# Kernel optimization log

Hardware: AMD Instinct MI355X
Metric: run time of the kernel (lower is better)

Reference implementation:

```python
import jax, jax.numpy as jnp
import numpy as np
import math

T = 4194304          # sequence length (e.g. minute bars)
MAX_KERNEL = 700     # number of EMA taps (from init_alpha=0.01)
INIT_ALPHA = 0.01


def setup_inputs() -> dict:
    key = jax.random.key(0)
    x = jax.random.normal(key, (T,), dtype=jnp.float32)
    # learnable logit-space alpha parameter: sigmoid(w_alpha) = init_alpha
    w_alpha = jnp.float32(math.log(INIT_ALPHA / (1.0 - INIT_ALPHA)))
    return {"x": x, "w_alpha": w_alpha}


def reference(x, w_alpha):
    K = MAX_KERNEL
    alpha = jax.nn.sigmoid(w_alpha)
    # exponential-decay kernel w_k = alpha * (1-alpha)^k, reconstructed each forward
    k = jnp.arange(K, dtype=x.dtype)
    kernel = alpha * jnp.power(1.0 - alpha, k)          # [K]
    w = kernel[::-1].reshape(1, 1, K)                   # flipped, [O=1, I=1, K]
    # causal left-pad with the first sample replicated (as in the torch module)
    left_pad = jnp.full((K - 1,), x[0], dtype=x.dtype)
    x_padded = jnp.concatenate([left_pad, x])[None, None, :]  # [1,1,T+K-1]
    # torch F.conv1d is cross-correlation; lax conv is too -> same math
    out = jax.lax.conv_general_dilated(
        x_padded, w,
        window_strides=(1,), padding="VALID",
        dimension_numbers=("NCH", "OIH", "NCH"),
    )
    return out[0, 0]  # [T]
```

## Files before the change

### kernel.cpp

```cpp
#include <hip/hip_runtime.h>
#include <math.h>


#define K_TAPS 700
#define NB     4096
#define EXT    2560
#define TOTAL  (NB + EXT)
#define BLOCK  256
#define LSEG   (TOTAL / BLOCK)

__global__ __launch_bounds__(BLOCK)
void diffema_kernel(const float* __restrict__ x,
                    const float* __restrict__ w_alpha,
                    float* __restrict__ out,
                    int T) {
    __shared__ float xs[TOTAL];
    __shared__ float ys[TOTAL];
    __shared__ float wP[BLOCK / 64];
    __shared__ float wV[BLOCK / 64];

    const int tid = threadIdx.x;
    const int bid = blockIdx.x;
    const int t0  = bid * NB;
    const int base = t0 - EXT;

    const float w     = w_alpha[0];
    const float alpha = 1.0f / (1.0f + expf(-w));
    const float c     = 1.0f - alpha;
    const float cK    = powf(c, (float)K_TAPS);
    const float cL    = powf(c, (float)LSEG);

    for (int j = tid; j < TOTAL; j += BLOCK) {
        int p = base + j;
        if (p < 0) p = 0;
        xs[j] = x[p];
    }
    __syncthreads();

    const int s0 = tid * LSEG;
    float v = 0.0f;
#pragma unroll
    for (int j = 0; j < LSEG; ++j) {
        v = c * v + alpha * xs[s0 + j];
    }

    float P = cL, V = v;
    const int lane = tid & 63;
#pragma unroll
    for (int d = 1; d < 64; d <<= 1) {
        float Pp = __shfl_up(P, d);
        float Vp = __shfl_up(V, d);
        if (lane >= d) {
            V = P * Vp + V;
            P = P * Pp;
        }
    }

    const int wave = tid >> 6;
    if (lane == 63) { wP[wave] = P; wV[wave] = V; }
    __syncthreads();

    float prefV = 0.0f;
    for (int k = 0; k < wave; ++k) {
        prefV = wP[k] * prefV + wV[k];
    }

    float Pex = __shfl_up(P, 1);
    float Vex = __shfl_up(V, 1);
    if (lane == 0) { Pex = 1.0f; Vex = 0.0f; }
    float s = Pex * prefV + Vex;

#pragma unroll
    for (int j = 0; j < LSEG; ++j) {
        s = c * s + alpha * xs[s0 + j];
        ys[s0 + j] = s;
    }
    __syncthreads();

#pragma unroll 4
    for (int j = tid; j < NB; j += BLOCK) {
        int q = EXT + j;
        out[t0 + j] = ys[q] - cK * ys[q - K_TAPS];
    }
}

extern "C" void kernel_launch(void* const* d_in, const int* in_sizes, int n_in,
                              void* d_out, int out_size, void* d_ws, size_t ws_size,
                              hipStream_t stream) {
    const float* x       = (const float*)d_in[0];
    const float* w_alpha = (const float*)d_in[1];
    float*       out     = (float*)d_out;
    const int T = in_sizes[0];

    const int nblocks = (T + NB - 1) / NB;
    diffema_kernel<<<nblocks, BLOCK, 0, stream>>>(x, w_alpha, out, T);
}
```

Measured before the change: 74.92 us.

## Apply tap-difference to input and keep EMA scan entirely in registers

The finite-tap EMA is recast as an infinite EMA of the differenced input u[t] = x[t] - c^K x[t-K], so a shorter warm-up window suffices. The kernel drops both shared-memory staging arrays: each thread loads its segment with float4 global loads straight into registers, runs a local scan, then corrects the scan with a multiplicative carry term before writing float4 outputs. Only the second half of threads write results. The costs are a second strided global read for x[t-K], more registers per thread, and a warm-up-to-output ratio of 1:1 where it was about 0.6:1 before, which means more redundant reads and compute per output.

```diff
diff --git a/kernel.cpp b/kernel.cpp
--- a/kernel.cpp
+++ b/kernel.cpp
@@ -3,84 +3,101 @@
 
 
 #define K_TAPS 700
-#define NB     4096
-#define EXT    2560
-#define TOTAL  (NB + EXT)
+#define W_WARM 2048
+#define NB     2048
+#define TOTAL  (W_WARM + NB)
 #define BLOCK  256
 #define LSEG   (TOTAL / BLOCK)
+#define NW     (BLOCK / 64)
 
 __global__ __launch_bounds__(BLOCK)
 void diffema_kernel(const float* __restrict__ x,
                     const float* __restrict__ w_alpha,
-                    float* __restrict__ out,
-                    int T) {
-    __shared__ float xs[TOTAL];
-    __shared__ float ys[TOTAL];
-    __shared__ float wP[BLOCK / 64];
-    __shared__ float wV[BLOCK / 64];
+                    float* __restrict__ out, int T) {
+    __shared__ float wP[NW], wV[NW];
 
-    const int tid = threadIdx.x;
-    const int bid = blockIdx.x;
-    const int t0  = bid * NB;
-    const int base = t0 - EXT;
+    const int tid  = threadIdx.x;
+    const int lane = tid & 63;
+    const int wave = tid >> 6;
+    const long t0   = (long)blockIdx.x * NB;
+    const long base = t0 - W_WARM;
+    const long segs = base + (long)tid * LSEG;
 
-    const float w     = w_alpha[0];
-    const float alpha = 1.0f / (1.0f + expf(-w));
+    const float wa    = w_alpha[0];
+    const float alpha = 1.0f / (1.0f + expf(-wa));
     const float c     = 1.0f - alpha;
     const float cK    = powf(c, (float)K_TAPS);
-    const float cL    = powf(c, (float)LSEG);
 
-    for (int j = tid; j < TOTAL; j += BLOCK) {
-        int p = base + j;
-        if (p < 0) p = 0;
-        xs[j] = x[p];
+    float u[LSEG];
+    {
+        float4 a[LSEG / 4], b[LSEG / 4];
+        const float x0 = x[0];
+#pragma unroll
+        for (int i = 0; i < LSEG / 4; ++i) {
+            long p = segs + 4 * i;
+            if (p >= 0) a[i] = *(const float4*)(x + p);
+            else        a[i] = make_float4(x0, x0, x0, x0);
+            long q = p - K_TAPS;
+            if (q >= 0) b[i] = *(const float4*)(x + q);
+            else        b[i] = make_float4(x0, x0, x0, x0);
+        }
+#pragma unroll
+        for (int i = 0; i < LSEG / 4; ++i) {
+            u[4 * i + 0] = fmaf(-cK, b[i].x, a[i].x);
+            u[4 * i + 1] = fmaf(-cK, b[i].y, a[i].y);
+            u[4 * i + 2] = fmaf(-cK, b[i].z, a[i].z);
+            u[4 * i + 3] = fmaf(-cK, b[i].w, a[i].w);
+        }
     }
-    __syncthreads();
 
-    const int s0 = tid * LSEG;
     float v = 0.0f;
 #pragma unroll
     for (int j = 0; j < LSEG; ++j) {
-        v = c * v + alpha * xs[s0 + j];
+        v = fmaf(c, v, alpha * u[j]);
+        u[j] = v;
     }
 
-    float P = cL, V = v;
-    const int lane = tid & 63;
+    float P = powf(c, (float)LSEG), V = v;
 #pragma unroll
     for (int d = 1; d < 64; d <<= 1) {
         float Pp = __shfl_up(P, d);
         float Vp = __shfl_up(V, d);
-        if (lane >= d) {
-            V = P * Vp + V;
-            P = P * Pp;
-        }
+        if (lane >= d) { V = fmaf(P, Vp, V); P *= Pp; }
     }
 
-    const int wave = tid >> 6;
     if (lane == 63) { wP[wave] = P; wV[wave] = V; }
     __syncthreads();
-
     float prefV = 0.0f;
-    for (int k = 0; k < wave; ++k) {
-        prefV = wP[k] * prefV + wV[k];
+#pragma unroll
+    for (int k = 0; k < NW - 1; ++k) {
+        if (k < wave) prefV = fmaf(wP[k], prefV, wV[k]);
     }
 
     float Pex = __shfl_up(P, 1);
     float Vex = __shfl_up(V, 1);
     if (lane == 0) { Pex = 1.0f; Vex = 0.0f; }
-    float s = Pex * prefV + Vex;
+    const float s = fmaf(Pex, prefV, Vex);
 
+    float m = s;
 #pragma unroll
     for (int j = 0; j < LSEG; ++j) {
-        s = c * s + alpha * xs[s0 + j];
-        ys[s0 + j] = s;
+        m *= c;
+        u[j] += m;
     }
-    __syncthreads();
 
-#pragma unroll 4
-    for (int j = tid; j < NB; j += BLOCK) {
-        int q = EXT + j;
-        out[t0 + j] = ys[q] - cK * ys[q - K_TAPS];
+    if (segs >= t0) {
+#pragma unroll
+        for (int i = 0; i < LSEG / 4; ++i) {
+            long p = segs + 4 * i;
+            if (p + 3 < (long)T) {
+                *(float4*)(out + p) =
+                    make_float4(u[4 * i + 0], u[4 * i + 1],
+                                u[4 * i + 2], u[4 * i + 3]);
+            } else {
+                for (int jj = 0; jj < 4; ++jj)
+                    if (p + jj < (long)T) out[p + jj] = u[4 * i + jj];
+            }
+        }
     }
 }
 
```

Measured after the change: 76.82 us. 2.5% more time.
